# Kernel optimization log

Measured on AMD Instinct MI355X. Metric: run time of the kernel, lower is better.

The kernel has to match this reference:

```python
import jax, jax.numpy as jnp
import numpy as np

BIG = 1e9

def _pairwise_iou(a, b):
    # a: [M,4] xywh GT, b: [A,4] xywh preds -> [M,A]
    tl = jnp.maximum(a[:, None, :2] - a[:, None, 2:] / 2, b[None, :, :2] - b[None, :, 2:] / 2)
    br = jnp.minimum(a[:, None, :2] + a[:, None, 2:] / 2, b[None, :, :2] + b[None, :, 2:] / 2)
    area_a = a[:, 2] * a[:, 3]
    area_b = b[:, 2] * b[:, 3]
    en = (tl < br).all(-1)
    area_i = jnp.prod(br - tl, -1) * en
    return area_i / (area_a[:, None] + area_b[None, :] - area_i + 1e-16)

def _bce_logits(x, t):
    # BCEWithLogits, reduction='none'
    return jnp.maximum(x, 0.0) - x * t + jnp.log1p(jnp.exp(-jnp.abs(x)))

def _forward(outputs, x_shifts, y_shifts, expanded_strides, labels, num_classes):
    C = num_classes
    strides = expanded_strides[0]                      # [A]
    xc = (x_shifts[0] + 0.5) * strides                 # anchor centers (pixels)
    yc = (y_shifts[0] + 0.5) * strides
    M = labels.shape[1]

    def assign(out_i, lab_i):
        # per-image SimOTA assignment (no_grad in original)
        bbox = out_i[:, :4]
        obj = out_i[:, 4]
        cls = out_i[:, 5:]
        gtb = lab_i[:, :4]
        gtc = lab_i[:, 4].astype(jnp.int32)
        valid = lab_i.sum(1) > 0                        # [M] padded GT mask
        # in-box test (strict, as min(deltas)>0)
        l = gtb[:, 0:1] - 0.5 * gtb[:, 2:3]
        r = gtb[:, 0:1] + 0.5 * gtb[:, 2:3]
        t = gtb[:, 1:2] - 0.5 * gtb[:, 3:4]
        bo = gtb[:, 1:2] + 0.5 * gtb[:, 3:4]
        in_boxes = (xc[None] > l) & (r > xc[None]) & (yc[None] > t) & (bo > yc[None]) & valid[:, None]
        # center-radius test (2.5 strides)
        rad = 2.5 * strides[None]
        in_ctr = ((xc[None] > gtb[:, 0:1] - rad) & (xc[None] < gtb[:, 0:1] + rad)
                  & (yc[None] > gtb[:, 1:2] - rad) & (yc[None] < gtb[:, 1:2] + rad)) & valid[:, None]
        fg = in_boxes.any(0) | in_ctr.any(0)            # [A] candidate anchors
        in_both = in_boxes & in_ctr                     # [M,A]

        ious = _pairwise_iou(gtb, bbox) * fg[None] * valid[:, None]   # [M,A]
        # pairwise BCE(sqrt(sigmoid(cls)*sigmoid(obj)), onehot) summed over classes
        p = jnp.sqrt(jax.nn.sigmoid(cls) * jax.nn.sigmoid(obj)[:, None])   # [A,C]
        logp = jnp.maximum(jnp.log(p), -100.0)
        log1mp = jnp.maximum(jnp.log1p(-p), -100.0)
        oh = jax.nn.one_hot(gtc, C, dtype=p.dtype)                          # [M,C]
        cls_cost = -(oh @ logp.T + log1mp.sum(-1)[None, :] - oh @ log1mp.T)  # [M,A]
        cost = cls_cost + 3.0 * (-jnp.log(ious + 1e-8)) + 100000.0 * (~in_both)
        cost = jnp.where(fg[None] & valid[:, None], cost, BIG)

        # dynamic-k: sum of top-10 ious per GT, truncated to int, min 1
        topk = jax.lax.top_k(ious, 10)[0]
        dyn_k = jnp.maximum(topk.sum(1).astype(jnp.int32), 1)               # [M]
        rank = jnp.argsort(jnp.argsort(cost, axis=1), axis=1)               # rank of each anchor per GT
        matching = (rank < dyn_k[:, None]) & valid[:, None] & fg[None]      # [M,A]
        # resolve anchors matched to >1 GT: keep min-cost GT
        amg = matching.sum(0)
        argmin_g = jnp.argmin(cost, axis=0)                                  # [A]
        oh_min = jnp.arange(M)[:, None] == argmin_g[None, :]
        matching = jnp.where(amg[None, :] > 1, oh_min, matching)
        fg_final = matching.any(0)                                           # [A]
        mgt = jnp.argmax(matching, axis=0)                                   # matched GT idx per anchor
        pious = (matching * ious).sum(0)                                     # [A]
        cls_t = jax.nn.one_hot(gtc[mgt], C, dtype=p.dtype) * pious[:, None]  # [A,C]
        reg_t = gtb[mgt]                                                     # [A,4]
        return cls_t, reg_t, fg_final, fg_final.sum()

    cls_t, reg_t, fg, nfg = jax.vmap(assign)(outputs, labels)
    cls_t = jax.lax.stop_gradient(cls_t)
    reg_t = jax.lax.stop_gradient(reg_t)
    fg = jax.lax.stop_gradient(fg)
    num_fg = jnp.maximum(jax.lax.stop_gradient(nfg.sum()).astype(jnp.float32), 1.0)

    bbox = outputs[..., :4].reshape(-1, 4)
    obj = outputs[..., 4]
    cls = outputs[..., 5:]
    tg = reg_t.reshape(-1, 4)
    fgf = fg.reshape(-1)
    # IOUloss ('iou' type): 1 - iou^2, masked to fg anchors
    tl = jnp.maximum(bbox[:, :2] - bbox[:, 2:] / 2, tg[:, :2] - tg[:, 2:] / 2)
    br = jnp.minimum(bbox[:, :2] + bbox[:, 2:] / 2, tg[:, :2] + tg[:, 2:] / 2)
    area_p = bbox[:, 2] * bbox[:, 3]
    area_g = tg[:, 2] * tg[:, 3]
    en = (tl < br).all(-1)
    area_i = jnp.prod(br - tl, -1) * en
    iou = area_i / (area_p + area_g - area_i + 1e-16)
    loss_iou = ((1.0 - iou ** 2) * fgf).sum() / num_fg
    loss_obj = _bce_logits(obj, fg.astype(obj.dtype)).sum() / num_fg
    loss_cls = (_bce_logits(cls, cls_t) * fg[..., None]).sum() / num_fg
    return 5.0 * loss_iou + loss_obj + loss_cls

def reference(outputs, x_shifts, y_shifts, expanded_strides, labels, num_classes):
    return _forward(outputs, x_shifts, y_shifts, expanded_strides, labels, num_classes)

def setup_inputs() -> dict:
    key = jax.random.key(0)
    B, C, M, IMG = 32, 80, 50, 640
    xs, ys, ss = [], [], []
    for s in (8, 16, 32):
        n = IMG // s
        gy, gx = np.meshgrid(np.arange(n), np.arange(n), indexing='ij')
        xs.append(gx.reshape(-1)); ys.append(gy.reshape(-1)); ss.append(np.full(n * n, s))
    x_shifts = jnp.asarray(np.concatenate(xs)[None], jnp.float32)
    y_shifts = jnp.asarray(np.concatenate(ys)[None], jnp.float32)
    expanded_strides = jnp.asarray(np.concatenate(ss)[None], jnp.float32)
    A = x_shifts.shape[1]  # 8400
    k1, k2, k3, k4, k5, k6, k7 = jax.random.split(key, 7)
    ctr = jax.random.uniform(k1, (B, A, 2), minval=0.0, maxval=float(IMG))
    wh = jax.random.uniform(k2, (B, A, 2), minval=8.0, maxval=128.0)
    logits = jax.random.normal(k3, (B, A, 1 + C))
    outputs = jnp.concatenate([ctr, wh, logits], -1).astype(jnp.float32)
    gctr = jax.random.uniform(k4, (B, M, 2), minval=32.0, maxval=float(IMG - 32))
    gwh = jax.random.uniform(k5, (B, M, 2), minval=16.0, maxval=160.0)
    gcls = jax.random.randint(k6, (B, M, 1), 0, C).astype(jnp.float32)
    ngt = jax.random.randint(k7, (B,), 5, M + 1)
    vmask = (jnp.arange(M)[None, :] < ngt[:, None])[..., None]
    labels = (jnp.concatenate([gctr, gwh, gcls], -1) * vmask).astype(jnp.float32)
    return {"outputs": outputs, "x_shifts": x_shifts, "y_shifts": y_shifts,
            "expanded_strides": expanded_strides, "labels": labels, "num_classes": C}
```

## Files before the change

kernel.cpp:

```cpp
#include <hip/hip_runtime.h>
#include <math.h>

#define TPB 256

#define LOG2E_F 1.4426950408889634f
#define LN2_F   0.6931471805599453f

__device__ __forceinline__ float sigmoidf_(float x){
    return 1.0f / (1.0f + expf(-x));
}

__device__ __forceinline__ float bce_(float x, float t){
    return fmaxf(x, 0.0f) - x * t + log1pf(expf(-fabsf(x)));
}

__device__ float iou_fn(float ax, float ay, float aw, float ah,
                        float bx, float by, float bw, float bh){
#pragma clang fp contract(off)
    float tlx = fmaxf(ax - aw * 0.5f, bx - bw * 0.5f);
    float tly = fmaxf(ay - ah * 0.5f, by - bh * 0.5f);
    float brx = fminf(ax + aw * 0.5f, bx + bw * 0.5f);
    float bry = fminf(ay + ah * 0.5f, by + bh * 0.5f);
    float area_a = aw * ah;
    float area_b = bw * bh;
    bool  en = (tlx < brx) && (tly < bry);
    float area_i = en ? (brx - tlx) * (bry - tly) : 0.0f;
    return area_i / (area_a + area_b - area_i + 1e-16f);
}

__device__ float cost_eval(float ox, float oy, float ow, float oh,
                           float clslogit, float so, float S1,
                           float xcv, float ycv, float rad,
                           float gx, float gy, float gw, float gh,
                           bool valid, bool fgflag){
#pragma clang fp contract(off)
    if (!(valid && fgflag)) return 1e9f;
    float raw = iou_fn(gx, gy, gw, gh, ox, oy, ow, oh);
    bool inb = (xcv > gx - 0.5f * gw) && (gx + 0.5f * gw > xcv) &&
               (ycv > gy - 0.5f * gh) && (gy + 0.5f * gh > ycv);
    bool inc = (xcv > gx - rad) && (xcv < gx + rad) &&
               (ycv > gy - rad) && (ycv < gy + rad);
    bool in_both = inb && inc;
    float pt = sqrtf(sigmoidf_(clslogit) * so);
    float logp = fmaxf(logf(pt), -100.0f);
    float l1mp = fmaxf(log1pf(-pt), -100.0f);
    float cls_cost = -(logp + S1 - l1mp);
    return cls_cost + 3.0f * (-logf(raw + 1e-8f)) + (in_both ? 0.0f : 100000.0f);
}

__global__ __launch_bounds__(TPB) void precompute_kernel(
    const float* __restrict__ outputs, const float* __restrict__ xs,
    const float* __restrict__ ys, const float* __restrict__ st,
    const float* __restrict__ labels,
    float* __restrict__ S1mp, float* __restrict__ sobj, float* __restrict__ obj4,
    float* __restrict__ bce0, float4* __restrict__ bb4,
    unsigned char* __restrict__ fgbuf,
    int* __restrict__ amg, unsigned int* __restrict__ firstm,
    float4* __restrict__ anc4,
    int A, int M, int C, int B, int nbA)
{
    __shared__ float slab[64 * 5];
    int t = threadIdx.x;
    int b = blockIdx.x / nbA;
    int chunk = blockIdx.x - b * nbA;
    int Ms = M < 64 ? M : 64;
    for (int i = t; i < Ms * 5; i += TPB) slab[i] = labels[(size_t)b * M * 5 + i];
    __syncthreads();

    int a = chunk * TPB + t;
    if (a >= A) return;
    size_t idx = (size_t)b * A + a;

    float s = st[a];
    float xcv = (xs[a] + 0.5f) * s;
    float ycv = (ys[a] + 0.5f) * s;
    float rad = 2.5f * s;
    if (b == 0) anc4[a] = make_float4(xcv, ycv, rad, 0.0f);

    amg[idx] = 0; firstm[idx] = 0xFFFFFFFFu;

    const float* o = outputs + idx * (size_t)(C + 5);
    float ox = o[0], oy = o[1], ow = o[2], ohh = o[3], x4 = o[4];
    bb4[idx] = make_float4(ox, oy, ow, ohh);

    float so = __builtin_amdgcn_rcpf(1.0f + __builtin_amdgcn_exp2f(-x4 * LOG2E_F));
    float s1 = 0.0f, b0 = 0.0f;
#pragma unroll 4
    for (int c = 0; c < C; c++){
        float xc = o[5 + c];
        float u = __builtin_amdgcn_exp2f(-xc * LOG2E_F);
        float tden = 1.0f + u;
        float sig = __builtin_amdgcn_rcpf(tden);
        float p = __builtin_amdgcn_sqrtf(sig * so);
        s1 += fmaxf(LN2_F * __builtin_amdgcn_logf(1.0f - p), -100.0f);
        b0 += xc + LN2_F * __builtin_amdgcn_logf(tden);
    }
    S1mp[idx] = s1; sobj[idx] = so; obj4[idx] = x4; bce0[idx] = b0;

    bool any = false;
    for (int m = 0; m < M && !any; m++){
        const float* lab = (m < Ms) ? (slab + m * 5)
                                    : (labels + ((size_t)b * M + m) * 5);
        float gx = lab[0], gy = lab[1], gw = lab[2], gh = lab[3], g4v = lab[4];
        if (!((gx + gy + gw + gh + g4v) > 0.0f)) continue;
        bool inb = (xcv > gx - 0.5f * gw) && (gx + 0.5f * gw > xcv) &&
                   (ycv > gy - 0.5f * gh) && (gy + 0.5f * gh > ycv);
        bool inc = (xcv > gx - rad) && (xcv < gx + rad) &&
                   (ycv > gy - rad) && (ycv < gy + rad);
        any = inb || inc;
    }
    fgbuf[idx] = any ? 1 : 0;
}

__global__ __launch_bounds__(TPB) void compact_kernel(
    const unsigned char* __restrict__ fgbuf, const float4* __restrict__ bb4,
    const float4* __restrict__ anc4, const float* __restrict__ S1mp,
    const float* __restrict__ sobj,
    float4* __restrict__ bbc, float4* __restrict__ ancc,
    float* __restrict__ sobc, int* __restrict__ aidxc, int* __restrict__ fgcnt,
    int A, int B)
{
    int b = blockIdx.x;
    int t = threadIdx.x;
    int lane = t & 63, wid = t >> 6;
    size_t base = (size_t)b * A;
    __shared__ int wtot[4];
    __shared__ int running;
    if (t == 0) running = 0;
    __syncthreads();
    for (int c0 = 0; c0 < A; c0 += TPB){
        int a = c0 + t;
        bool flag = (a < A) && (fgbuf[base + a] != 0);
        unsigned long long mask = __ballot(flag);
        int prefix = __popcll(mask & ((1ull << lane) - 1ull));
        int tot = __popcll(mask);
        if (lane == 0) wtot[wid] = tot;
        __syncthreads();
        int off = running;
        for (int w = 0; w < wid; w++) off += wtot[w];
        if (flag){
            int pos = off + prefix;
            bbc[base + pos] = bb4[base + a];
            float4 an = anc4[a];
            an.w = S1mp[base + a];
            ancc[base + pos] = an;
            sobc[base + pos] = sobj[base + a];
            aidxc[base + pos] = a;
        }
        __syncthreads();
        if (t == 0) running += wtot[0] + wtot[1] + wtot[2] + wtot[3];
        __syncthreads();
    }
    if (t == 0) fgcnt[b] = running;
}

__global__ __launch_bounds__(TPB) void assign_kernel(
    const float* __restrict__ outputs,
    const float* __restrict__ labels,
    const float4* __restrict__ bbc, const float4* __restrict__ ancc,
    const float* __restrict__ sobc, const int* __restrict__ aidxc,
    const int* __restrict__ fgcnt,
    int* __restrict__ amg, unsigned int* __restrict__ firstm,
    int A, int M, int C, int B)
{
    int b = blockIdx.x / M;
    int m = blockIdx.x - b * M;
    int t = threadIdx.x;
    int lane = t & 63, wid = t >> 6;

    const float* lab = labels + ((size_t)b * M + m) * 5;
    float gx = lab[0], gy = lab[1], gw = lab[2], gh = lab[3], g4 = lab[4];
    int  gc = (int)g4;
    bool valid = (gx + gy + gw + gh + g4) > 0.0f;
    if (!valid) return;

    const size_t base = (size_t)b * A;
    const float* outb = outputs + base * (size_t)(C + 5);
    int n = fgcnt[b];

    float gl = gx - 0.5f * gw, gr = gx + 0.5f * gw;
    float gt_ = gy - 0.5f * gh, gb_ = gy + 0.5f * gh;

    float tv[10];
    float cv[10]; int ci[10];
#pragma unroll
    for (int j = 0; j < 10; j++){ tv[j] = -2.0f; cv[j] = 4e9f; ci[j] = 0x7fffffff; }
    int nib = 0;

    for (int i = t; i < n; i += TPB){
        float4 bb = bbc[base + i];
        float4 an = ancc[base + i];

        float v = iou_fn(gx, gy, gw, gh, bb.x, bb.y, bb.z, bb.w);
        if (v > tv[9]){
            tv[9] = v;
#pragma unroll
            for (int j = 9; j > 0; j--){
                if (tv[j] > tv[j-1]){ float tm = tv[j]; tv[j] = tv[j-1]; tv[j-1] = tm; }
            }
        }

        bool inb = (an.x > gl) && (gr > an.x) && (an.y > gt_) && (gb_ > an.y);
        bool inc = (an.x > gx - an.z) && (an.x < gx + an.z) &&
                   (an.y > gy - an.z) && (an.y < gy + an.z);
        if (inb && inc){
            nib++;
            int a = aidxc[base + i];
            float c = cost_eval(bb.x, bb.y, bb.z, bb.w,
                                outb[(size_t)a * (C + 5) + 5 + gc],
                                sobc[base + i], an.w,
                                an.x, an.y, an.z, gx, gy, gw, gh, true, true);
            if (c < cv[9] || (c == cv[9] && a < ci[9])){
                cv[9] = c; ci[9] = a;
#pragma unroll
                for (int j = 9; j > 0; j--){
                    if (cv[j] < cv[j-1] || (cv[j] == cv[j-1] && ci[j] < ci[j-1])){
                        float tf = cv[j]; cv[j] = cv[j-1]; cv[j-1] = tf;
                        int  ti = ci[j]; ci[j] = ci[j-1]; ci[j-1] = ti;
                    }
                }
            }
        }
    }

    __shared__ int snib[4];
    int nr = nib;
#pragma unroll
    for (int off = 32; off; off >>= 1) nr += __shfl_xor(nr, off);
    if (lane == 0) snib[wid] = nr;
    __syncthreads();
    int total_nib = snib[0] + snib[1] + snib[2] + snib[3];

    __shared__ float swv[2][4];
    __shared__ int   swi[2][4];

    float topsum = 0.0f;
    for (int k = 0; k < 10; k++){
        float v = tv[0];
        int who = t;
#pragma unroll
        for (int off = 32; off; off >>= 1){
            float v2 = __shfl_xor(v, off);
            int   w2 = __shfl_xor(who, off);
            if (v2 > v || (v2 == v && w2 < who)){ v = v2; who = w2; }
        }
        int slot = k & 1;
        if (lane == 0){ swv[slot][wid] = v; swi[slot][wid] = who; }
        __syncthreads();
        float gv = swv[slot][0]; int gwho = swi[slot][0];
#pragma unroll
        for (int w = 1; w < 4; w++){
            float v2 = swv[slot][w]; int w2 = swi[slot][w];
            if (v2 > gv || (v2 == gv && w2 < gwho)){ gv = v2; gwho = w2; }
        }
        topsum += fmaxf(gv, 0.0f);
        if (t == gwho){
#pragma unroll
            for (int j = 0; j < 9; j++) tv[j] = tv[j+1];
            tv[9] = -2.0f;
        }
    }
    int dyn_k = (int)topsum;
    if (dyn_k < 1) dyn_k = 1;
    if (dyn_k > 10) dyn_k = 10;

    if (dyn_k > total_nib){
#pragma unroll
        for (int j = 0; j < 10; j++){ cv[j] = 4e9f; ci[j] = 0x7fffffff; }
        for (int i = t; i < n; i += TPB){
            float4 bb = bbc[base + i];
            float4 an = ancc[base + i];
            int a = aidxc[base + i];
            float c = cost_eval(bb.x, bb.y, bb.z, bb.w,
                                outb[(size_t)a * (C + 5) + 5 + gc],
                                sobc[base + i], an.w,
                                an.x, an.y, an.z, gx, gy, gw, gh, true, true);
            if (c < cv[9] || (c == cv[9] && a < ci[9])){
                cv[9] = c; ci[9] = a;
#pragma unroll
                for (int j = 9; j > 0; j--){
                    if (cv[j] < cv[j-1] || (cv[j] == cv[j-1] && ci[j] < ci[j-1])){
                        float tf = cv[j]; cv[j] = cv[j-1]; cv[j-1] = tf;
                        int  ti = ci[j]; ci[j] = ci[j-1]; ci[j-1] = ti;
                    }
                }
            }
        }
    }
    __syncthreads();

    for (int k = 0; k < dyn_k; k++){
        float v = cv[0]; int ai = ci[0];
#pragma unroll
        for (int off = 32; off; off >>= 1){
            float v2 = __shfl_xor(v, off);
            int   a2 = __shfl_xor(ai, off);
            if (v2 < v || (v2 == v && a2 < ai)){ v = v2; ai = a2; }
        }
        int slot = k & 1;
        if (lane == 0){ swv[slot][wid] = v; swi[slot][wid] = ai; }
        __syncthreads();
        float gv = swv[slot][0]; int gai = swi[slot][0];
#pragma unroll
        for (int w = 1; w < 4; w++){
            float v2 = swv[slot][w]; int a2 = swi[slot][w];
            if (v2 < gv || (v2 == gv && a2 < gai)){ gv = v2; gai = a2; }
        }
        if (gv >= 1e8f) break;
        if (cv[0] == gv && ci[0] == gai){
            atomicAdd(&amg[base + gai], 1);
            atomicMin(&firstm[base + gai], (unsigned)m);
#pragma unroll
            for (int j = 0; j < 9; j++){ cv[j] = cv[j+1]; ci[j] = ci[j+1]; }
            cv[9] = 4e9f; ci[9] = 0x7fffffff;
        }
    }
}

__global__ __launch_bounds__(TPB) void finalize_kernel(
    const float* __restrict__ outputs,
    const float4* __restrict__ anc4,
    const float* __restrict__ labels, const float* __restrict__ S1mp,
    const float* __restrict__ sobj, const float* __restrict__ obj4,
    const float* __restrict__ bce0, const float4* __restrict__ bb4,
    const int* __restrict__ amg, const unsigned int* __restrict__ firstm,
    float* __restrict__ pacc, int A, int M, int C, int B)
{
    int idx = blockIdx.x * TPB + threadIdx.x;
    int BA = B * A;
    float s_iou = 0.0f, s_obj = 0.0f, s_cls = 0.0f, s_nfg = 0.0f;
    if (idx < BA){
        int b = idx / A;
        int a = idx - b * A;
        int cnt = amg[idx];
        bool fgf = cnt >= 1;
        s_obj = bce_(obj4[idx], fgf ? 1.0f : 0.0f);
        if (fgf){
            float4 bb = bb4[idx];
            int mgt = (int)firstm[idx];
            if (cnt > 1){
                float S1 = S1mp[idx], so = sobj[idx];
                float4 an = anc4[a];
                const float* orow = outputs + (size_t)idx * (C + 5);
                float best = 1e30f; int bi = 0;
                for (int m = 0; m < M; m++){
                    const float* lab = labels + ((size_t)b * M + m) * 5;
                    float gx = lab[0], gy = lab[1], gw = lab[2], gh = lab[3], g4 = lab[4];
                    bool vld = (gx + gy + gw + gh + g4) > 0.0f;
                    float c = cost_eval(bb.x, bb.y, bb.z, bb.w, orow[5 + (int)g4],
                                        so, S1, an.x, an.y, an.z,
                                        gx, gy, gw, gh, vld, true);
                    if (c < best){ best = c; bi = m; }
                }
                mgt = bi;
            }
            const float* lab = labels + ((size_t)b * M + mgt) * 5;
            float pious = iou_fn(lab[0], lab[1], lab[2], lab[3], bb.x, bb.y, bb.z, bb.w);
            s_iou = 1.0f - pious * pious;
            s_nfg = 1.0f;
            int gc = (int)lab[4];
            s_cls = bce0[idx] - outputs[(size_t)idx * (C + 5) + 5 + gc] * pious;
        }
    }
    for (int off = 32; off > 0; off >>= 1){
        s_iou += __shfl_down(s_iou, off);
        s_obj += __shfl_down(s_obj, off);
        s_cls += __shfl_down(s_cls, off);
        s_nfg += __shfl_down(s_nfg, off);
    }
    __shared__ float red[4][4];
    int lane = threadIdx.x & 63, wid = threadIdx.x >> 6;
    if (lane == 0){
        red[wid][0] = s_iou; red[wid][1] = s_obj;
        red[wid][2] = s_cls; red[wid][3] = s_nfg;
    }
    __syncthreads();
    if (threadIdx.x < 4){
        float v = red[0][threadIdx.x] + red[1][threadIdx.x]
                + red[2][threadIdx.x] + red[3][threadIdx.x];
        pacc[(size_t)blockIdx.x * 4 + threadIdx.x] = v;
    }
}

__global__ __launch_bounds__(TPB) void combine_kernel(
    const float* __restrict__ pacc, int nblk, float* __restrict__ out)
{
    float s0 = 0.0f, s1 = 0.0f, s2 = 0.0f, s3 = 0.0f;
    for (int i = threadIdx.x; i < nblk; i += TPB){
        s0 += pacc[(size_t)i * 4 + 0];
        s1 += pacc[(size_t)i * 4 + 1];
        s2 += pacc[(size_t)i * 4 + 2];
        s3 += pacc[(size_t)i * 4 + 3];
    }
    for (int off = 32; off > 0; off >>= 1){
        s0 += __shfl_down(s0, off);
        s1 += __shfl_down(s1, off);
        s2 += __shfl_down(s2, off);
        s3 += __shfl_down(s3, off);
    }
    __shared__ float red[4][4];
    int lane = threadIdx.x & 63, wid = threadIdx.x >> 6;
    if (lane == 0){ red[wid][0] = s0; red[wid][1] = s1; red[wid][2] = s2; red[wid][3] = s3; }
    __syncthreads();
    if (threadIdx.x == 0){
        float t0 = red[0][0] + red[1][0] + red[2][0] + red[3][0];
        float t1 = red[0][1] + red[1][1] + red[2][1] + red[3][1];
        float t2 = red[0][2] + red[1][2] + red[2][2] + red[3][2];
        float t3 = red[0][3] + red[1][3] + red[2][3] + red[3][3];
        float nfg = fmaxf(t3, 1.0f);
        out[0] = (5.0f * t0 + t1 + t2) / nfg;
    }
}

extern "C" void kernel_launch(void* const* d_in, const int* in_sizes, int n_in,
                              void* d_out, int out_size, void* d_ws, size_t ws_size,
                              hipStream_t stream)
{
    const float* outputs = (const float*)d_in[0];
    const float* xs      = (const float*)d_in[1];
    const float* ys      = (const float*)d_in[2];
    const float* st      = (const float*)d_in[3];
    const float* labels  = (const float*)d_in[4];

    const int C = 80;
    int A = in_sizes[1];
    int B = in_sizes[0] / (A * (C + 5));
    int M = in_sizes[4] / (B * 5);
    int BA = B * A;
    int nb  = (BA + TPB - 1) / TPB;
    int nbA = (A + TPB - 1) / TPB;

    char* w = (char*)d_ws;
    auto carve = [&](size_t bytes) -> char* {
        char* p = w;
        w += (bytes + 255) & ~(size_t)255;
        return p;
    };
    float* S1mp = (float*)carve((size_t)BA * 4);
    float* sobj = (float*)carve((size_t)BA * 4);
    float* obj4 = (float*)carve((size_t)BA * 4);
    float* bce0 = (float*)carve((size_t)BA * 4);
    float4* bb4 = (float4*)carve((size_t)BA * 16);
    int*   amg  = (int*)carve((size_t)BA * 4);
    unsigned int* firstm = (unsigned int*)carve((size_t)BA * 4);
    unsigned char* fgbuf = (unsigned char*)carve((size_t)BA);
    float4* anc4 = (float4*)carve((size_t)A * 16);
    float* pacc = (float*)carve((size_t)nb * 4 * 4);
    float4* bbc  = (float4*)carve((size_t)BA * 16);
    float4* ancc = (float4*)carve((size_t)BA * 16);
    float*  sobc = (float*)carve((size_t)BA * 4);
    int*    aidxc= (int*)carve((size_t)BA * 4);
    int*    fgcnt= (int*)carve((size_t)B * 4);

    precompute_kernel<<<dim3(B * nbA), dim3(TPB), 0, stream>>>(
        outputs, xs, ys, st, labels, S1mp, sobj, obj4, bce0,
        bb4, fgbuf, amg, firstm, anc4, A, M, C, B, nbA);
    compact_kernel<<<dim3(B), dim3(TPB), 0, stream>>>(
        fgbuf, bb4, anc4, S1mp, sobj, bbc, ancc, sobc, aidxc, fgcnt, A, B);
    assign_kernel<<<dim3(B * M), dim3(TPB), 0, stream>>>(
        outputs, labels, bbc, ancc, sobc, aidxc, fgcnt,
        amg, firstm, A, M, C, B);
    finalize_kernel<<<dim3(nb), dim3(TPB), 0, stream>>>(
        outputs, anc4, labels, S1mp, sobj, obj4, bce0,
        bb4, amg, firstm, pacc, A, M, C, B);
    combine_kernel<<<dim3(1), dim3(TPB), 0, stream>>>(pacc, nb, (float*)d_out);
}
```

Measured before the change: 344.4 us.

## Precompute per-anchor class terms with one wavefront per row for coalesced loads

The precompute kernel now gives each row of outputs (85 floats) to a whole 64-lane wavefront. The lanes read the row in a coalesced way, compute the class terms in parallel, and combine them with a shuffle reduction. Before, each thread looped over its own strided row, so memory access was uncoalesced. The finalize kernel's objectness BCE also switches to fast exp2/log intrinsics. The change adds a serial loop over 64 rows per wave and shuffle overhead, and it hardcodes 85 columns (C=80).

Result: no change. 345.5 us (+0.3%).

```diff
diff --git a/kernel.cpp b/kernel.cpp
--- a/kernel.cpp
+++ b/kernel.cpp
@@ -10,8 +10,9 @@
     return 1.0f / (1.0f + expf(-x));
 }
 
-__device__ __forceinline__ float bce_(float x, float t){
-    return fmaxf(x, 0.0f) - x * t + log1pf(expf(-fabsf(x)));
+__device__ __forceinline__ float bce_fast(float x, float t){
+    float u = __builtin_amdgcn_exp2f(-fabsf(x) * LOG2E_F);
+    return fmaxf(x, 0.0f) - x * t + LN2_F * __builtin_amdgcn_logf(1.0f + u);
 }
 
 __device__ float iou_fn(float ax, float ay, float aw, float ah,
@@ -63,11 +64,55 @@
     int t = threadIdx.x;
     int b = blockIdx.x / nbA;
     int chunk = blockIdx.x - b * nbA;
+    int a0 = chunk * TPB;
     int Ms = M < 64 ? M : 64;
     for (int i = t; i < Ms * 5; i += TPB) slab[i] = labels[(size_t)b * M * 5 + i];
-    __syncthreads();
-
-    int a = chunk * TPB + t;
+
+    int lane = t & 63, wid = t >> 6;
+    int rbase = a0 + wid * 64;
+    for (int i = 0; i < 64; ++i){
+        int r = rbase + i;
+        if (r >= A) break;
+        size_t idx = (size_t)b * A + r;
+        const float* row = outputs + idx * (size_t)(C + 5);
+        float x1 = row[lane];
+        float x2 = (lane < 21) ? row[64 + lane] : 0.0f;
+
+        float x4 = __shfl(x1, 4);
+        float so = __builtin_amdgcn_rcpf(1.0f + __builtin_amdgcn_exp2f(-x4 * LOG2E_F));
+
+        float s1c = 0.0f, b0c = 0.0f;
+        if (lane >= 5){
+            float u = __builtin_amdgcn_exp2f(-x1 * LOG2E_F);
+            float tden = 1.0f + u;
+            float sig = __builtin_amdgcn_rcpf(tden);
+            float p = __builtin_amdgcn_sqrtf(sig * so);
+            s1c = fmaxf(LN2_F * __builtin_amdgcn_logf(1.0f - p), -100.0f);
+            b0c = x1 + LN2_F * __builtin_amdgcn_logf(tden);
+        }
+        if (lane < 21){
+            float u = __builtin_amdgcn_exp2f(-x2 * LOG2E_F);
+            float tden = 1.0f + u;
+            float sig = __builtin_amdgcn_rcpf(tden);
+            float p = __builtin_amdgcn_sqrtf(sig * so);
+            s1c += fmaxf(LN2_F * __builtin_amdgcn_logf(1.0f - p), -100.0f);
+            b0c += x2 + LN2_F * __builtin_amdgcn_logf(tden);
+        }
+#pragma unroll
+        for (int off = 32; off; off >>= 1){
+            s1c += __shfl_xor(s1c, off);
+            b0c += __shfl_xor(b0c, off);
+        }
+        float bx = __shfl(x1, 0), by_ = __shfl(x1, 1);
+        float bw_ = __shfl(x1, 2), bh_ = __shfl(x1, 3);
+        if (lane == 0){
+            S1mp[idx] = s1c; bce0[idx] = b0c; sobj[idx] = so; obj4[idx] = x4;
+            bb4[idx] = make_float4(bx, by_, bw_, bh_);
+        }
+    }
+    __syncthreads();
+
+    int a = a0 + t;
     if (a >= A) return;
     size_t idx = (size_t)b * A + a;
 
@@ -78,24 +123,6 @@
     if (b == 0) anc4[a] = make_float4(xcv, ycv, rad, 0.0f);
 
     amg[idx] = 0; firstm[idx] = 0xFFFFFFFFu;
-
-    const float* o = outputs + idx * (size_t)(C + 5);
-    float ox = o[0], oy = o[1], ow = o[2], ohh = o[3], x4 = o[4];
-    bb4[idx] = make_float4(ox, oy, ow, ohh);
-
-    float so = __builtin_amdgcn_rcpf(1.0f + __builtin_amdgcn_exp2f(-x4 * LOG2E_F));
-    float s1 = 0.0f, b0 = 0.0f;
-#pragma unroll 4
-    for (int c = 0; c < C; c++){
-        float xc = o[5 + c];
-        float u = __builtin_amdgcn_exp2f(-xc * LOG2E_F);
-        float tden = 1.0f + u;
-        float sig = __builtin_amdgcn_rcpf(tden);
-        float p = __builtin_amdgcn_sqrtf(sig * so);
-        s1 += fmaxf(LN2_F * __builtin_amdgcn_logf(1.0f - p), -100.0f);
-        b0 += xc + LN2_F * __builtin_amdgcn_logf(tden);
-    }
-    S1mp[idx] = s1; sobj[idx] = so; obj4[idx] = x4; bce0[idx] = b0;
 
     bool any = false;
     for (int m = 0; m < M && !any; m++){
@@ -334,7 +361,7 @@
         int a = idx - b * A;
         int cnt = amg[idx];
         bool fgf = cnt >= 1;
-        s_obj = bce_(obj4[idx], fgf ? 1.0f : 0.0f);
+        s_obj = bce_fast(obj4[idx], fgf ? 1.0f : 0.0f);
         if (fgf){
             float4 bb = bb4[idx];
             int mgt = (int)firstm[idx];
```

## Stage output rows in LDS, split class loop, parallelize foreground compaction

Applied to the files above, without the earlier changes.

The precompute kernel now stages 64-row tiles of the prediction tensor in shared memory with coalesced float4 loads and splits each row's 80-class loop across four lanes, reduced with shuffles. The single-block-per-image serial compaction is replaced by per-chunk counts, a small scan kernel and a fully parallel scatter kernel. The finalize objectness BCE also switches to hardware exp2/log intrinsics. The tile layout hardcodes 85 floats per row (C=80), so other class counts would break, and an extra kernel launch is added.

Result: faster. 278.0 us (-19.3%).

```diff
diff --git a/kernel.cpp b/kernel.cpp
--- a/kernel.cpp
+++ b/kernel.cpp
@@ -10,8 +10,9 @@
     return 1.0f / (1.0f + expf(-x));
 }
 
-__device__ __forceinline__ float bce_(float x, float t){
-    return fmaxf(x, 0.0f) - x * t + log1pf(expf(-fabsf(x)));
+__device__ __forceinline__ float bce_fast(float x, float t){
+    float u = __builtin_amdgcn_exp2f(-fabsf(x) * LOG2E_F);
+    return fmaxf(x, 0.0f) - x * t + LN2_F * __builtin_amdgcn_logf(1.0f + u);
 }
 
 __device__ float iou_fn(float ax, float ay, float aw, float ah,
@@ -56,102 +57,141 @@
     float* __restrict__ bce0, float4* __restrict__ bb4,
     unsigned char* __restrict__ fgbuf,
     int* __restrict__ amg, unsigned int* __restrict__ firstm,
-    float4* __restrict__ anc4,
+    float4* __restrict__ anc4, int* __restrict__ chunkcnt,
     int A, int M, int C, int B, int nbA)
 {
+    __shared__ float tile[64 * 85];
     __shared__ float slab[64 * 5];
+    __shared__ int wtot[4];
     int t = threadIdx.x;
     int b = blockIdx.x / nbA;
     int chunk = blockIdx.x - b * nbA;
+    int a0 = chunk * TPB;
     int Ms = M < 64 ? M : 64;
     for (int i = t; i < Ms * 5; i += TPB) slab[i] = labels[(size_t)b * M * 5 + i];
+
+    int row = t >> 2, q = t & 3;
+    for (int s = 0; s < 4; ++s){
+        int r0 = a0 + s * 64;
+        int nrows = A - r0; if (nrows > 64) nrows = 64;
+        if (nrows <= 0) break;
+        int nf = nrows * 85;
+        const float* g = outputs + ((size_t)b * A + r0) * 85;
+        if ((((size_t)g) & 15) == 0){
+            int n4 = nf >> 2;
+            const float4* g4 = (const float4*)g;
+            float4* l4 = (float4*)tile;
+            for (int i = t; i < n4; i += TPB) l4[i] = g4[i];
+            for (int i = (n4 << 2) + t; i < nf; i += TPB) tile[i] = g[i];
+        } else {
+            for (int i = t; i < nf; i += TPB) tile[i] = g[i];
+        }
+        __syncthreads();
+        if (row < nrows){
+            const float* rw = tile + row * 85;
+            size_t idx = (size_t)b * A + r0 + row;
+            float x4 = rw[4];
+            float so = __builtin_amdgcn_rcpf(1.0f + __builtin_amdgcn_exp2f(-x4 * LOG2E_F));
+            float s1c = 0.0f, b0c = 0.0f;
+            const float* cls = rw + 5 + q * 20;
+#pragma unroll 5
+            for (int k = 0; k < 20; ++k){
+                float xc = cls[k];
+                float u = __builtin_amdgcn_exp2f(-xc * LOG2E_F);
+                float tden = 1.0f + u;
+                float sig = __builtin_amdgcn_rcpf(tden);
+                float p = __builtin_amdgcn_sqrtf(sig * so);
+                s1c += fmaxf(LN2_F * __builtin_amdgcn_logf(1.0f - p), -100.0f);
+                b0c += xc + LN2_F * __builtin_amdgcn_logf(tden);
+            }
+            s1c += __shfl_xor(s1c, 1); s1c += __shfl_xor(s1c, 2);
+            b0c += __shfl_xor(b0c, 1); b0c += __shfl_xor(b0c, 2);
+            if (q == 0){
+                S1mp[idx] = s1c; bce0[idx] = b0c; sobj[idx] = so; obj4[idx] = x4;
+                bb4[idx] = make_float4(rw[0], rw[1], rw[2], rw[3]);
+            }
+        }
+        __syncthreads();
+    }
+
+    int a = a0 + t;
+    int lane = t & 63, wid = t >> 6;
+    bool flag = false;
+    if (a < A){
+        size_t idx = (size_t)b * A + a;
+        float s = st[a];
+        float xcv = (xs[a] + 0.5f) * s;
+        float ycv = (ys[a] + 0.5f) * s;
+        float rad = 2.5f * s;
+        if (b == 0) anc4[a] = make_float4(xcv, ycv, rad, 0.0f);
+        amg[idx] = 0; firstm[idx] = 0xFFFFFFFFu;
+
+        bool any = false;
+        for (int m = 0; m < M && !any; m++){
+            const float* lab = (m < Ms) ? (slab + m * 5)
+                                        : (labels + ((size_t)b * M + m) * 5);
+            float gx = lab[0], gy = lab[1], gw = lab[2], gh = lab[3], g4v = lab[4];
+            if (!((gx + gy + gw + gh + g4v) > 0.0f)) continue;
+            bool inb = (xcv > gx - 0.5f * gw) && (gx + 0.5f * gw > xcv) &&
+                       (ycv > gy - 0.5f * gh) && (gy + 0.5f * gh > ycv);
+            bool inc = (xcv > gx - rad) && (xcv < gx + rad) &&
+                       (ycv > gy - rad) && (ycv < gy + rad);
+            any = inb || inc;
+        }
+        fgbuf[idx] = any ? 1 : 0;
+        flag = any;
+    }
+    unsigned long long mask = __ballot(flag);
+    if (lane == 0) wtot[wid] = __popcll(mask);
     __syncthreads();
-
-    int a = chunk * TPB + t;
-    if (a >= A) return;
-    size_t idx = (size_t)b * A + a;
-
-    float s = st[a];
-    float xcv = (xs[a] + 0.5f) * s;
-    float ycv = (ys[a] + 0.5f) * s;
-    float rad = 2.5f * s;
-    if (b == 0) anc4[a] = make_float4(xcv, ycv, rad, 0.0f);
-
-    amg[idx] = 0; firstm[idx] = 0xFFFFFFFFu;
-
-    const float* o = outputs + idx * (size_t)(C + 5);
-    float ox = o[0], oy = o[1], ow = o[2], ohh = o[3], x4 = o[4];
-    bb4[idx] = make_float4(ox, oy, ow, ohh);
-
-    float so = __builtin_amdgcn_rcpf(1.0f + __builtin_amdgcn_exp2f(-x4 * LOG2E_F));
-    float s1 = 0.0f, b0 = 0.0f;
-#pragma unroll 4
-    for (int c = 0; c < C; c++){
-        float xc = o[5 + c];
-        float u = __builtin_amdgcn_exp2f(-xc * LOG2E_F);
-        float tden = 1.0f + u;
-        float sig = __builtin_amdgcn_rcpf(tden);
-        float p = __builtin_amdgcn_sqrtf(sig * so);
-        s1 += fmaxf(LN2_F * __builtin_amdgcn_logf(1.0f - p), -100.0f);
-        b0 += xc + LN2_F * __builtin_amdgcn_logf(tden);
-    }
-    S1mp[idx] = s1; sobj[idx] = so; obj4[idx] = x4; bce0[idx] = b0;
-
-    bool any = false;
-    for (int m = 0; m < M && !any; m++){
-        const float* lab = (m < Ms) ? (slab + m * 5)
-                                    : (labels + ((size_t)b * M + m) * 5);
-        float gx = lab[0], gy = lab[1], gw = lab[2], gh = lab[3], g4v = lab[4];
-        if (!((gx + gy + gw + gh + g4v) > 0.0f)) continue;
-        bool inb = (xcv > gx - 0.5f * gw) && (gx + 0.5f * gw > xcv) &&
-                   (ycv > gy - 0.5f * gh) && (gy + 0.5f * gh > ycv);
-        bool inc = (xcv > gx - rad) && (xcv < gx + rad) &&
-                   (ycv > gy - rad) && (ycv < gy + rad);
-        any = inb || inc;
-    }
-    fgbuf[idx] = any ? 1 : 0;
-}
-
-__global__ __launch_bounds__(TPB) void compact_kernel(
+    if (t == 0) chunkcnt[b * nbA + chunk] = wtot[0] + wtot[1] + wtot[2] + wtot[3];
+}
+
+__global__ __launch_bounds__(64) void scan_kernel(
+    const int* __restrict__ chunkcnt, int* __restrict__ chunkoff,
+    int* __restrict__ fgcnt, int B, int nbA)
+{
+    int b = threadIdx.x + blockIdx.x * 64;
+    if (b >= B) return;
+    int run = 0;
+    for (int c = 0; c < nbA; c++){
+        chunkoff[b * nbA + c] = run;
+        run += chunkcnt[b * nbA + c];
+    }
+    fgcnt[b] = run;
+}
+
+__global__ __launch_bounds__(TPB) void scatter_kernel(
     const unsigned char* __restrict__ fgbuf, const float4* __restrict__ bb4,
     const float4* __restrict__ anc4, const float* __restrict__ S1mp,
-    const float* __restrict__ sobj,
+    const float* __restrict__ sobj, const int* __restrict__ chunkoff,
     float4* __restrict__ bbc, float4* __restrict__ ancc,
-    float* __restrict__ sobc, int* __restrict__ aidxc, int* __restrict__ fgcnt,
-    int A, int B)
-{
-    int b = blockIdx.x;
+    float* __restrict__ sobc, int* __restrict__ aidxc,
+    int A, int nbA)
+{
     int t = threadIdx.x;
+    int b = blockIdx.x / nbA;
+    int chunk = blockIdx.x - b * nbA;
+    int a = chunk * TPB + t;
+    size_t base = (size_t)b * A;
+    bool flag = (a < A) && (fgbuf[base + a] != 0);
     int lane = t & 63, wid = t >> 6;
-    size_t base = (size_t)b * A;
+    unsigned long long mask = __ballot(flag);
+    int prefix = __popcll(mask & ((1ull << lane) - 1ull));
     __shared__ int wtot[4];
-    __shared__ int running;
-    if (t == 0) running = 0;
+    if (lane == 0) wtot[wid] = __popcll(mask);
     __syncthreads();
-    for (int c0 = 0; c0 < A; c0 += TPB){
-        int a = c0 + t;
-        bool flag = (a < A) && (fgbuf[base + a] != 0);
-        unsigned long long mask = __ballot(flag);
-        int prefix = __popcll(mask & ((1ull << lane) - 1ull));
-        int tot = __popcll(mask);
-        if (lane == 0) wtot[wid] = tot;
-        __syncthreads();
-        int off = running;
-        for (int w = 0; w < wid; w++) off += wtot[w];
-        if (flag){
-            int pos = off + prefix;
-            bbc[base + pos] = bb4[base + a];
-            float4 an = anc4[a];
-            an.w = S1mp[base + a];
-            ancc[base + pos] = an;
-            sobc[base + pos] = sobj[base + a];
-            aidxc[base + pos] = a;
-        }
-        __syncthreads();
-        if (t == 0) running += wtot[0] + wtot[1] + wtot[2] + wtot[3];
-        __syncthreads();
-    }
-    if (t == 0) fgcnt[b] = running;
+    int off = chunkoff[b * nbA + chunk];
+    for (int w = 0; w < wid; w++) off += wtot[w];
+    if (flag){
+        int pos = off + prefix;
+        bbc[base + pos] = bb4[base + a];
+        float4 an = anc4[a];
+        an.w = S1mp[base + a];
+        ancc[base + pos] = an;
+        sobc[base + pos] = sobj[base + a];
+        aidxc[base + pos] = a;
+    }
 }
 
 __global__ __launch_bounds__(TPB) void assign_kernel(
@@ -334,7 +374,7 @@
         int a = idx - b * A;
         int cnt = amg[idx];
         bool fgf = cnt >= 1;
-        s_obj = bce_(obj4[idx], fgf ? 1.0f : 0.0f);
+        s_obj = bce_fast(obj4[idx], fgf ? 1.0f : 0.0f);
         if (fgf){
             float4 bb = bb4[idx];
             int mgt = (int)firstm[idx];
@@ -451,12 +491,17 @@
     float*  sobc = (float*)carve((size_t)BA * 4);
     int*    aidxc= (int*)carve((size_t)BA * 4);
     int*    fgcnt= (int*)carve((size_t)B * 4);
+    int*    chunkcnt = (int*)carve((size_t)B * nbA * 4);
+    int*    chunkoff = (int*)carve((size_t)B * nbA * 4);
 
     precompute_kernel<<<dim3(B * nbA), dim3(TPB), 0, stream>>>(
         outputs, xs, ys, st, labels, S1mp, sobj, obj4, bce0,
-        bb4, fgbuf, amg, firstm, anc4, A, M, C, B, nbA);
-    compact_kernel<<<dim3(B), dim3(TPB), 0, stream>>>(
-        fgbuf, bb4, anc4, S1mp, sobj, bbc, ancc, sobc, aidxc, fgcnt, A, B);
+        bb4, fgbuf, amg, firstm, anc4, chunkcnt, A, M, C, B, nbA);
+    scan_kernel<<<dim3((B + 63) / 64), dim3(64), 0, stream>>>(
+        chunkcnt, chunkoff, fgcnt, B, nbA);
+    scatter_kernel<<<dim3(B * nbA), dim3(TPB), 0, stream>>>(
+        fgbuf, bb4, anc4, S1mp, sobj, chunkoff,
+        bbc, ancc, sobc, aidxc, A, nbA);
     assign_kernel<<<dim3(B * M), dim3(TPB), 0, stream>>>(
         outputs, labels, bbc, ancc, sobc, aidxc, fgcnt,
         amg, firstm, A, M, C, B);
```
